# Kernel optimization log

Measured on AMD Instinct MI355X. Metric: run time of the kernel, lower is better.

## Reference

```python
import jax, jax.numpy as jnp
import numpy as np

N_NODES = 50000
N_EDGES = 800000
IN_DIM, HID_DIM, OUT_DIM = 768, 512, 256


def setup_inputs() -> dict:
    key = jax.random.key(0)
    k1, k2, k3, k4, k5 = jax.random.split(key, 5)
    x = jax.random.normal(k1, (N_NODES, IN_DIM), dtype=jnp.float32)
    edge_index = jax.random.randint(k2, (2, N_EDGES), 0, N_NODES, dtype=jnp.int64)
    # GCNConv params (glorot-ish init)
    W1 = jax.random.normal(k3, (IN_DIM, HID_DIM), dtype=jnp.float32) / np.sqrt(IN_DIM)
    b1 = jnp.zeros((HID_DIM,), dtype=jnp.float32)
    W2 = jax.random.normal(k4, (HID_DIM, OUT_DIM), dtype=jnp.float32) / np.sqrt(HID_DIM)
    b2 = jnp.zeros((OUT_DIM,), dtype=jnp.float32)
    return {"x": x, "edge_index": edge_index, "W1": W1, "b1": b1, "W2": W2, "b2": b2}


def gcn_conv(x, W, b, src, dst, n_nodes):
    """PyG GCNConv: add self-loops, symmetric degree norm, linear, scatter-add, bias."""
    h = x @ W  # [N, F_out]
    loop = jnp.arange(n_nodes, dtype=src.dtype)
    s = jnp.concatenate([src, loop])  # sources incl. self-loops
    d = jnp.concatenate([dst, loop])  # destinations incl. self-loops
    deg = jax.ops.segment_sum(jnp.ones_like(d, dtype=h.dtype), d, num_segments=n_nodes)
    dinv = jnp.where(deg > 0, jax.lax.rsqrt(deg), 0.0)
    norm = dinv[s] * dinv[d]  # [E+N]
    msgs = h[s] * norm[:, None]  # gather + scale (largest intermediate)
    out = jax.ops.segment_sum(msgs, d, num_segments=n_nodes)  # scatter-add
    return out + b


def reference(x, edge_index, W1, b1, W2, b2):
    src, dst = edge_index[0], edge_index[1]
    n = x.shape[0]
    h = gcn_conv(x, W1, b1, src, dst, n)
    h = jax.nn.relu(h)  # dropout is identity in eval mode
    out = gcn_conv(h, W2, b2, src, dst, n)
    return out
```

## Files before the change

### kernel.cpp

```cpp
#include <hip/hip_runtime.h>

#define N_NODES 50000
#define N_EDGES 800000
#define IN_DIM  768
#define HID_DIM 512
#define OUT_DIM 256
#define M_PAD   50048

typedef __attribute__((ext_vector_type(8))) short shortx8;
typedef __attribute__((ext_vector_type(4))) short shortx4;
typedef __attribute__((ext_vector_type(4))) float floatx4;

#define AS1 __attribute__((address_space(1)))
#define AS3 __attribute__((address_space(3)))

__device__ __forceinline__ unsigned short f2bf_rne(float f) {
    unsigned int u = __float_as_uint(f);
    unsigned int r = u + 0x7FFFu + ((u >> 16) & 1u);
    return (unsigned short)(r >> 16);
}
__device__ __forceinline__ float bf2f(unsigned short h) {
    return __uint_as_float(((unsigned int)h) << 16);
}

__global__ void count_deg_kernel(const int* __restrict__ dst, int* __restrict__ deg,
                                 int n_edges) {
    int e = blockIdx.x * blockDim.x + threadIdx.x;
    if (e < n_edges) atomicAdd(&deg[dst[e]], 1);
}

#define SCAN_B 256
#define N_SCAN_BLOCKS ((N_NODES + SCAN_B - 1) / SCAN_B)

__global__ void block_sum_kernel(const int* __restrict__ deg, int* __restrict__ partials,
                                 int n) {
    __shared__ int sm[SCAN_B];
    int i = blockIdx.x * SCAN_B + threadIdx.x;
    sm[threadIdx.x] = (i < n) ? deg[i] : 0;
    __syncthreads();
    for (int off = SCAN_B / 2; off > 0; off >>= 1) {
        if (threadIdx.x < off) sm[threadIdx.x] += sm[threadIdx.x + off];
        __syncthreads();
    }
    if (threadIdx.x == 0) partials[blockIdx.x] = sm[0];
}

__global__ void scan_partials_kernel(const int* __restrict__ partials,
                                     int* __restrict__ bases, int nb) {
    __shared__ int sm[SCAN_B];
    int v = (threadIdx.x < nb) ? partials[threadIdx.x] : 0;
    sm[threadIdx.x] = v;
    __syncthreads();
    for (int off = 1; off < SCAN_B; off <<= 1) {
        int t = (threadIdx.x >= off) ? sm[threadIdx.x - off] : 0;
        __syncthreads();
        sm[threadIdx.x] += t;
        __syncthreads();
    }
    if (threadIdx.x < nb) bases[threadIdx.x] = sm[threadIdx.x] - v;
}

__global__ void finalize_scan_kernel(const int* __restrict__ deg, const int* __restrict__ bases,
                                     int* __restrict__ offsets, int* __restrict__ cursor,
                                     float* __restrict__ dinv, int n) {
    __shared__ int sm[SCAN_B];
    int i = blockIdx.x * SCAN_B + threadIdx.x;
    int v = (i < n) ? deg[i] : 0;
    sm[threadIdx.x] = v;
    __syncthreads();
    for (int off = 1; off < SCAN_B; off <<= 1) {
        int t = (threadIdx.x >= off) ? sm[threadIdx.x - off] : 0;
        __syncthreads();
        sm[threadIdx.x] += t;
        __syncthreads();
    }
    if (i < n) {
        int incl = bases[blockIdx.x] + sm[threadIdx.x];
        int o = incl - v;
        offsets[i] = o;
        cursor[i]  = o;
        dinv[i]    = rsqrtf((float)(v + 1));
        if (i == n - 1) offsets[n] = incl;
    }
}

__global__ void fill_csr_kernel(const int* __restrict__ src, const int* __restrict__ dst,
                                int* __restrict__ cursor, int* __restrict__ csr_src,
                                int n_edges) {
    int e = blockIdx.x * blockDim.x + threadIdx.x;
    if (e < n_edges) {
        int p = atomicAdd(&cursor[dst[e]], 1);
        csr_src[p] = src[e];
    }
}

__global__ void convert_split_kernel(const float* __restrict__ x,
                                     unsigned short* __restrict__ xhi,
                                     unsigned short* __restrict__ xlo,
                                     long long n4) {
    long long i = (long long)blockIdx.x * blockDim.x + threadIdx.x;
    if (i >= n4) return;
    float4 v = *reinterpret_cast<const float4*>(x + i * 4);
    ushort4 h, l;
    h.x = f2bf_rne(v.x); l.x = f2bf_rne(v.x - bf2f(h.x));
    h.y = f2bf_rne(v.y); l.y = f2bf_rne(v.y - bf2f(h.y));
    h.z = f2bf_rne(v.z); l.z = f2bf_rne(v.z - bf2f(h.z));
    h.w = f2bf_rne(v.w); l.w = f2bf_rne(v.w - bf2f(h.w));
    *reinterpret_cast<ushort4*>(xhi + i * 4) = h;
    *reinterpret_cast<ushort4*>(xlo + i * 4) = l;
}

__global__ void transpose_split_kernel(const float* __restrict__ W,
                                       unsigned short* __restrict__ Whi,
                                       unsigned short* __restrict__ Wlo,
                                       int K, int N) {
    __shared__ float tile[32][33];
    int n0 = blockIdx.x * 32, k0 = blockIdx.y * 32;
    int tx = threadIdx.x, ty = threadIdx.y;
    tile[ty][tx] = W[(size_t)(k0 + ty) * N + n0 + tx];
    __syncthreads();
    float v = tile[tx][ty];
    unsigned short h = f2bf_rne(v);
    size_t o = (size_t)(n0 + ty) * K + k0 + tx;
    Whi[o] = h;
    Wlo[o] = f2bf_rne(v - bf2f(h));
}

#define GBK 32

__global__ __launch_bounds__(256)
void gemm_bf16x3_kernel(const unsigned short* __restrict__ Ahi,
                        const unsigned short* __restrict__ Alo,
                        const unsigned short* __restrict__ Bhi,
                        const unsigned short* __restrict__ Blo,
                        const float* __restrict__ dinv,
                        unsigned short* __restrict__ C,
                        int M, int N, int K) {
    __shared__ __align__(16) unsigned short As[2][2][128][GBK];
    __shared__ __align__(16) unsigned short Bs[2][2][128][GBK];

    const int tid  = threadIdx.x;
    const int lane = tid & 63;
    const int wave = tid >> 6;

    const int gx   = gridDim.x;
    const int nwg  = gx * gridDim.y;
    const int blin = blockIdx.y * gx + blockIdx.x;
    const int qq   = nwg >> 3, rr = nwg & 7;
    const int xcd  = blin & 7, idx = blin >> 3;
    const int tt   = (xcd < rr ? xcd * (qq + 1) : rr * (qq + 1) + (xcd - rr) * qq) + idx;
    const int rowBase = (tt / gx) * 128;
    const int colBase = (tt % gx) * 128;

    const unsigned short* gsrc =
        (wave == 0) ? Ahi : (wave == 1) ? Alo : (wave == 2) ? Bhi : Blo;
    unsigned short* l0 =
        (wave == 0) ? &As[0][0][0][0] : (wave == 1) ? &As[0][1][0][0]
      : (wave == 2) ? &Bs[0][0][0][0] : &Bs[0][1][0][0];
    unsigned short* l1 = l0 + 2 * 128 * GBK;
    const int rbase = (wave < 2) ? rowBase : colBase;
    const int cg = ((lane & 3) ^ ((lane >> 3) & 3)) * 8;
    const size_t laneRowOff = (size_t)(rbase + (lane >> 2)) * K + cg;

    const int m0  = (wave & 1) * 64;
    const int n0  = (wave >> 1) * 64;
    const int r16 = lane & 15;
    const int kswz = ((lane >> 4) ^ ((r16 >> 1) & 3)) * 8;

    floatx4 acc[4][4] = {};

#pragma unroll
    for (int j = 0; j < 8; j++) {
        const unsigned short* g = gsrc + laneRowOff + (size_t)(j * 16) * K;
        __builtin_amdgcn_global_load_lds((const AS1 void*)g,
                                         (AS3 void*)(l0 + j * 16 * GBK), 16, 0, 0);
    }
    __syncthreads();

    int cur = 0;
    for (int k0 = 0; k0 < K; k0 += GBK) {
        if (k0 + GBK < K) {
            unsigned short* dstp = cur ? l0 : l1;
#pragma unroll
            for (int j = 0; j < 8; j++) {
                const unsigned short* g =
                    gsrc + laneRowOff + (size_t)(j * 16) * K + (k0 + GBK);
                __builtin_amdgcn_global_load_lds((const AS1 void*)g,
                                                 (AS3 void*)(dstp + j * 16 * GBK),
                                                 16, 0, 0);
            }
        }

        shortx8 ah[4], al[4], bh[4], bv[4];
#pragma unroll
        for (int i = 0; i < 4; i++) {
            ah[i] = *reinterpret_cast<const shortx8*>(&As[cur][0][m0 + i * 16 + r16][kswz]);
            al[i] = *reinterpret_cast<const shortx8*>(&As[cur][1][m0 + i * 16 + r16][kswz]);
            bh[i] = *reinterpret_cast<const shortx8*>(&Bs[cur][0][n0 + i * 16 + r16][kswz]);
            bv[i] = *reinterpret_cast<const shortx8*>(&Bs[cur][1][n0 + i * 16 + r16][kswz]);
        }
#pragma unroll
        for (int i = 0; i < 4; i++)
#pragma unroll
            for (int j = 0; j < 4; j++) {
                acc[i][j] = __builtin_amdgcn_mfma_f32_16x16x32_bf16(ah[i], bh[j], acc[i][j], 0, 0, 0);
                acc[i][j] = __builtin_amdgcn_mfma_f32_16x16x32_bf16(ah[i], bv[j], acc[i][j], 0, 0, 0);
                acc[i][j] = __builtin_amdgcn_mfma_f32_16x16x32_bf16(al[i], bh[j], acc[i][j], 0, 0, 0);
            }
        __syncthreads();
        cur ^= 1;
    }

#pragma unroll
    for (int i = 0; i < 4; i++) {
        int rsub = rowBase + m0 + i * 16 + (lane >> 4) * 4;
#pragma unroll
        for (int j = 0; j < 4; j++) {
            int col = colBase + n0 + j * 16 + r16;
#pragma unroll
            for (int r = 0; r < 4; r++) {
                int row = rsub + r;
                if (row < M) C[(size_t)row * N + col] = f2bf_rne(acc[i][j][r] * dinv[row]);
            }
        }
    }
}

__global__ __launch_bounds__(64)
void aggregate1_kernel(const unsigned short* __restrict__ hs, const int* __restrict__ offsets,
                       const int* __restrict__ csr_src, const float* __restrict__ dinv,
                       const float* __restrict__ bias,
                       unsigned short* __restrict__ yhi,
                       unsigned short* __restrict__ ylo) {
    __shared__ int idxs[64];
    const int node = blockIdx.x;
    const int c = threadIdx.x * 8;
    const unsigned short* hp = hs + c;

    float acc[8];
    {
        shortx8 r = *reinterpret_cast<const shortx8*>(hp + (size_t)node * HID_DIM);
#pragma unroll
        for (int q = 0; q < 8; q++) acc[q] = bf2f((unsigned short)r[q]);
    }
    int beg = offsets[node], end = offsets[node + 1];
    for (int base = beg; base < end; base += 64) {
        int cnt = min(64, end - base);
        __syncthreads();
        if ((int)threadIdx.x < cnt) idxs[threadIdx.x] = csr_src[base + threadIdx.x];
        __syncthreads();
        int j = 0;
        for (; j + 8 <= cnt; j += 8) {
            shortx8 r0 = *reinterpret_cast<const shortx8*>(hp + (size_t)idxs[j + 0] * HID_DIM);
            shortx8 r1 = *reinterpret_cast<const shortx8*>(hp + (size_t)idxs[j + 1] * HID_DIM);
            shortx8 r2 = *reinterpret_cast<const shortx8*>(hp + (size_t)idxs[j + 2] * HID_DIM);
            shortx8 r3 = *reinterpret_cast<const shortx8*>(hp + (size_t)idxs[j + 3] * HID_DIM);
            shortx8 r4 = *reinterpret_cast<const shortx8*>(hp + (size_t)idxs[j + 4] * HID_DIM);
            shortx8 r5 = *reinterpret_cast<const shortx8*>(hp + (size_t)idxs[j + 5] * HID_DIM);
            shortx8 r6 = *reinterpret_cast<const shortx8*>(hp + (size_t)idxs[j + 6] * HID_DIM);
            shortx8 r7 = *reinterpret_cast<const shortx8*>(hp + (size_t)idxs[j + 7] * HID_DIM);
#pragma unroll
            for (int q = 0; q < 8; q++)
                acc[q] += ((bf2f((unsigned short)r0[q]) + bf2f((unsigned short)r1[q]))
                         + (bf2f((unsigned short)r2[q]) + bf2f((unsigned short)r3[q])))
                        + ((bf2f((unsigned short)r4[q]) + bf2f((unsigned short)r5[q]))
                         + (bf2f((unsigned short)r6[q]) + bf2f((unsigned short)r7[q])));
        }
        for (; j < cnt; j++) {
            shortx8 r = *reinterpret_cast<const shortx8*>(hp + (size_t)idxs[j] * HID_DIM);
#pragma unroll
            for (int q = 0; q < 8; q++) acc[q] += bf2f((unsigned short)r[q]);
        }
    }
    float dv = dinv[node];
    floatx4 b0 = *reinterpret_cast<const floatx4*>(bias + c);
    floatx4 b1 = *reinterpret_cast<const floatx4*>(bias + c + 4);
    shortx8 h8, l8;
#pragma unroll
    for (int q = 0; q < 8; q++) {
        float bq = (q < 4) ? b0[q] : b1[q - 4];
        float o = fmaxf(acc[q] * dv + bq, 0.f);
        unsigned short h = f2bf_rne(o);
        h8[q] = (short)h;
        l8[q] = (short)f2bf_rne(o - bf2f(h));
    }
    __builtin_nontemporal_store(h8, reinterpret_cast<shortx8*>(yhi + (size_t)node * HID_DIM + c));
    __builtin_nontemporal_store(l8, reinterpret_cast<shortx8*>(ylo + (size_t)node * HID_DIM + c));
}

__global__ __launch_bounds__(64)
void aggregate2_kernel(const unsigned short* __restrict__ hs, const int* __restrict__ offsets,
                       const int* __restrict__ csr_src, const float* __restrict__ dinv,
                       const float* __restrict__ bias, float* __restrict__ out) {
    __shared__ int idxs[64];
    const int node = blockIdx.x;
    const int c = threadIdx.x * 4;
    const unsigned short* hp = hs + c;

    float acc[4];
    {
        shortx4 r = *reinterpret_cast<const shortx4*>(hp + (size_t)node * OUT_DIM);
#pragma unroll
        for (int q = 0; q < 4; q++) acc[q] = bf2f((unsigned short)r[q]);
    }
    int beg = offsets[node], end = offsets[node + 1];
    for (int base = beg; base < end; base += 64) {
        int cnt = min(64, end - base);
        __syncthreads();
        if ((int)threadIdx.x < cnt) idxs[threadIdx.x] = csr_src[base + threadIdx.x];
        __syncthreads();
        int j = 0;
        for (; j + 8 <= cnt; j += 8) {
            shortx4 r0 = *reinterpret_cast<const shortx4*>(hp + (size_t)idxs[j + 0] * OUT_DIM);
            shortx4 r1 = *reinterpret_cast<const shortx4*>(hp + (size_t)idxs[j + 1] * OUT_DIM);
            shortx4 r2 = *reinterpret_cast<const shortx4*>(hp + (size_t)idxs[j + 2] * OUT_DIM);
            shortx4 r3 = *reinterpret_cast<const shortx4*>(hp + (size_t)idxs[j + 3] * OUT_DIM);
            shortx4 r4 = *reinterpret_cast<const shortx4*>(hp + (size_t)idxs[j + 4] * OUT_DIM);
            shortx4 r5 = *reinterpret_cast<const shortx4*>(hp + (size_t)idxs[j + 5] * OUT_DIM);
            shortx4 r6 = *reinterpret_cast<const shortx4*>(hp + (size_t)idxs[j + 6] * OUT_DIM);
            shortx4 r7 = *reinterpret_cast<const shortx4*>(hp + (size_t)idxs[j + 7] * OUT_DIM);
#pragma unroll
            for (int q = 0; q < 4; q++)
                acc[q] += ((bf2f((unsigned short)r0[q]) + bf2f((unsigned short)r1[q]))
                         + (bf2f((unsigned short)r2[q]) + bf2f((unsigned short)r3[q])))
                        + ((bf2f((unsigned short)r4[q]) + bf2f((unsigned short)r5[q]))
                         + (bf2f((unsigned short)r6[q]) + bf2f((unsigned short)r7[q])));
        }
        for (; j < cnt; j++) {
            shortx4 r = *reinterpret_cast<const shortx4*>(hp + (size_t)idxs[j] * OUT_DIM);
#pragma unroll
            for (int q = 0; q < 4; q++) acc[q] += bf2f((unsigned short)r[q]);
        }
    }
    float dv = dinv[node];
    floatx4 b = *reinterpret_cast<const floatx4*>(bias + c);
    floatx4 o = { acc[0] * dv + b[0], acc[1] * dv + b[1],
                  acc[2] * dv + b[2], acc[3] * dv + b[3] };
    __builtin_nontemporal_store(o, reinterpret_cast<floatx4*>(out + (size_t)node * OUT_DIM + c));
}

extern "C" void kernel_launch(void* const* d_in, const int* in_sizes, int n_in,
                              void* d_out, int out_size, void* d_ws, size_t ws_size,
                              hipStream_t stream) {
    const float* x    = (const float*)d_in[0];
    const int*   edge = (const int*)d_in[1];
    const float* W1   = (const float*)d_in[2];
    const float* b1   = (const float*)d_in[3];
    const float* W2   = (const float*)d_in[4];
    const float* b2   = (const float*)d_in[5];
    float* out = (float*)d_out;

    const int* src = edge;
    const int* dst = edge + N_EDGES;

    char*  ws  = (char*)d_ws;
    size_t off = 0;
    auto alloc = [&](size_t bytes) -> void* {
        void* p = ws + off;
        off += (bytes + 255) & ~(size_t)255;
        return p;
    };
    int*   deg      = (int*)alloc((size_t)N_NODES * 4);
    float* dinv     = (float*)alloc((size_t)N_NODES * 4);
    int*   offsets  = (int*)alloc((size_t)(N_NODES + 1) * 4);
    int*   cursor   = (int*)alloc((size_t)N_NODES * 4);
    int*   csr_src  = (int*)alloc((size_t)N_EDGES * 4);
    int*   partials = (int*)alloc((size_t)N_SCAN_BLOCKS * 4);
    int*   bases    = (int*)alloc((size_t)N_SCAN_BLOCKS * 4);
    unsigned short* xhi   = (unsigned short*)alloc((size_t)M_PAD * IN_DIM * 2);
    unsigned short* xlo   = (unsigned short*)alloc((size_t)M_PAD * IN_DIM * 2);
    unsigned short* w1thi = (unsigned short*)alloc((size_t)HID_DIM * IN_DIM * 2);
    unsigned short* w1tlo = (unsigned short*)alloc((size_t)HID_DIM * IN_DIM * 2);
    unsigned short* w2thi = (unsigned short*)alloc((size_t)OUT_DIM * HID_DIM * 2);
    unsigned short* w2tlo = (unsigned short*)alloc((size_t)OUT_DIM * HID_DIM * 2);
    unsigned short* hs = (unsigned short*)alloc((size_t)N_NODES * HID_DIM * 2);

    unsigned short* y1hi = xhi;
    unsigned short* y1lo = xlo;

    hipMemsetAsync(deg, 0, (size_t)N_NODES * 4, stream);
    count_deg_kernel<<<(N_EDGES + 255) / 256, 256, 0, stream>>>(dst, deg, N_EDGES);
    block_sum_kernel<<<N_SCAN_BLOCKS, SCAN_B, 0, stream>>>(deg, partials, N_NODES);
    scan_partials_kernel<<<1, SCAN_B, 0, stream>>>(partials, bases, N_SCAN_BLOCKS);
    finalize_scan_kernel<<<N_SCAN_BLOCKS, SCAN_B, 0, stream>>>(deg, bases, offsets, cursor,
                                                               dinv, N_NODES);
    fill_csr_kernel<<<(N_EDGES + 255) / 256, 256, 0, stream>>>(src, dst, cursor, csr_src, N_EDGES);

    long long n4x = (long long)N_NODES * IN_DIM / 4;
    convert_split_kernel<<<(int)((n4x + 255) / 256), 256, 0, stream>>>(x, xhi, xlo, n4x);
    transpose_split_kernel<<<dim3(HID_DIM / 32, IN_DIM / 32), dim3(32, 32), 0, stream>>>(
        W1, w1thi, w1tlo, IN_DIM, HID_DIM);
    transpose_split_kernel<<<dim3(OUT_DIM / 32, HID_DIM / 32), dim3(32, 32), 0, stream>>>(
        W2, w2thi, w2tlo, HID_DIM, OUT_DIM);

    gemm_bf16x3_kernel<<<dim3(HID_DIM / 128, M_PAD / 128), 256, 0, stream>>>(
        xhi, xlo, w1thi, w1tlo, dinv, hs, N_NODES, HID_DIM, IN_DIM);
    aggregate1_kernel<<<N_NODES, 64, 0, stream>>>(
        hs, offsets, csr_src, dinv, b1, y1hi, y1lo);

    gemm_bf16x3_kernel<<<dim3(OUT_DIM / 128, M_PAD / 128), 256, 0, stream>>>(
        y1hi, y1lo, w2thi, w2tlo, dinv, hs, N_NODES, OUT_DIM, HID_DIM);
    aggregate2_kernel<<<N_NODES, 64, 0, stream>>>(
        hs, offsets, csr_src, dinv, b2, out);
}
```

Baseline: 796.8 us.

## Load B operand directly from global into registers, halve LDS footprint

The GEMM no longer stages the weight (B) tiles through shared memory. Each wave reads its B fragments straight from global/L2 into registers every k-step, and all four waves now share the A hi/lo staging loads. Shared memory use is halved, and launch bounds request 3 blocks per CU to raise occupancy. The trade-off is that global B loads sit on the critical path with no prefetch or double-buffering, and each B element is read by two waves. That adds latency and L2 traffic, which higher occupancy may or may not hide.

```diff
diff --git a/kernel.cpp b/kernel.cpp
--- a/kernel.cpp
+++ b/kernel.cpp
@@ -128,7 +128,7 @@
 
 #define GBK 32
 
-__global__ __launch_bounds__(256)
+__global__ __launch_bounds__(256, 3)
 void gemm_bf16x3_kernel(const unsigned short* __restrict__ Ahi,
                         const unsigned short* __restrict__ Alo,
                         const unsigned short* __restrict__ Bhi,
@@ -137,7 +137,6 @@
                         unsigned short* __restrict__ C,
                         int M, int N, int K) {
     __shared__ __align__(16) unsigned short As[2][2][128][GBK];
-    __shared__ __align__(16) unsigned short Bs[2][2][128][GBK];
 
     const int tid  = threadIdx.x;
     const int lane = tid & 63;
@@ -152,52 +151,63 @@
     const int rowBase = (tt / gx) * 128;
     const int colBase = (tt % gx) * 128;
 
-    const unsigned short* gsrc =
-        (wave == 0) ? Ahi : (wave == 1) ? Alo : (wave == 2) ? Bhi : Blo;
-    unsigned short* l0 =
-        (wave == 0) ? &As[0][0][0][0] : (wave == 1) ? &As[0][1][0][0]
-      : (wave == 2) ? &Bs[0][0][0][0] : &Bs[0][1][0][0];
-    unsigned short* l1 = l0 + 2 * 128 * GBK;
-    const int rbase = (wave < 2) ? rowBase : colBase;
+    const int hl = wave >> 1;
+    const int rq = (wave & 1) * 64;
+    const unsigned short* gsrc = hl ? Alo : Ahi;
+    unsigned short* lbase = &As[0][hl][rq][0];
     const int cg = ((lane & 3) ^ ((lane >> 3) & 3)) * 8;
-    const size_t laneRowOff = (size_t)(rbase + (lane >> 2)) * K + cg;
+    const size_t laneRowOff = (size_t)(rowBase + rq + (lane >> 2)) * K + cg;
 
     const int m0  = (wave & 1) * 64;
     const int n0  = (wave >> 1) * 64;
     const int r16 = lane & 15;
+    const int kq  = (lane >> 4) * 8;
     const int kswz = ((lane >> 4) ^ ((r16 >> 1) & 3)) * 8;
 
+    const unsigned short* bph[4];
+    const unsigned short* bpl[4];
+#pragma unroll
+    for (int j = 0; j < 4; j++) {
+        int col = colBase + n0 + j * 16 + r16;
+        bph[j] = Bhi + (size_t)col * K + kq;
+        bpl[j] = Blo + (size_t)col * K + kq;
+    }
+
     floatx4 acc[4][4] = {};
 
 #pragma unroll
-    for (int j = 0; j < 8; j++) {
+    for (int j = 0; j < 4; j++) {
         const unsigned short* g = gsrc + laneRowOff + (size_t)(j * 16) * K;
         __builtin_amdgcn_global_load_lds((const AS1 void*)g,
-                                         (AS3 void*)(l0 + j * 16 * GBK), 16, 0, 0);
+                                         (AS3 void*)(lbase + j * 16 * GBK), 16, 0, 0);
     }
     __syncthreads();
 
     int cur = 0;
     for (int k0 = 0; k0 < K; k0 += GBK) {
         if (k0 + GBK < K) {
-            unsigned short* dstp = cur ? l0 : l1;
-#pragma unroll
-            for (int j = 0; j < 8; j++) {
+            unsigned short* dstb = lbase + (cur ^ 1) * (2 * 128 * GBK);
+#pragma unroll
+            for (int j = 0; j < 4; j++) {
                 const unsigned short* g =
                     gsrc + laneRowOff + (size_t)(j * 16) * K + (k0 + GBK);
                 __builtin_amdgcn_global_load_lds((const AS1 void*)g,
-                                                 (AS3 void*)(dstp + j * 16 * GBK),
+                                                 (AS3 void*)(dstb + j * 16 * GBK),
                                                  16, 0, 0);
             }
         }
 
-        shortx8 ah[4], al[4], bh[4], bv[4];
+        shortx8 bh[4], bv[4];
+#pragma unroll
+        for (int j = 0; j < 4; j++) {
+            bh[j] = *reinterpret_cast<const shortx8*>(bph[j] + k0);
+            bv[j] = *reinterpret_cast<const shortx8*>(bpl[j] + k0);
+        }
+        shortx8 ah[4], al[4];
 #pragma unroll
         for (int i = 0; i < 4; i++) {
             ah[i] = *reinterpret_cast<const shortx8*>(&As[cur][0][m0 + i * 16 + r16][kswz]);
             al[i] = *reinterpret_cast<const shortx8*>(&As[cur][1][m0 + i * 16 + r16][kswz]);
-            bh[i] = *reinterpret_cast<const shortx8*>(&Bs[cur][0][n0 + i * 16 + r16][kswz]);
-            bv[i] = *reinterpret_cast<const shortx8*>(&Bs[cur][1][n0 + i * 16 + r16][kswz]);
         }
 #pragma unroll
         for (int i = 0; i < 4; i++)
```

New measurement: 876.7 us. 1.1x slower.

## Prefetch two K-tiles ahead in the bf16x3 GEMM using explicit waitcnt barriers

Applied to the files above, without the earlier changes.

Restructures the GEMM main loop so global-to-LDS loads run two K-tiles ahead instead of one. Fragments are read from LDS into registers first, then a barrier frees that buffer so the next-next tile can be issued into it while the MFMAs run. Partial vmcnt waits replace full __syncthreads, MFMA sections get raised wave priority, and launch bounds request two workgroups per CU. The hand-written waitcnt counts assume exactly 8 outstanding loads per stage, and the occupancy hint may force register spilling.

```diff
diff --git a/kernel.cpp b/kernel.cpp
--- a/kernel.cpp
+++ b/kernel.cpp
@@ -128,7 +128,7 @@
 
 #define GBK 32
 
-__global__ __launch_bounds__(256)
+__global__ __launch_bounds__(256, 2)
 void gemm_bf16x3_kernel(const unsigned short* __restrict__ Ahi,
                         const unsigned short* __restrict__ Alo,
                         const unsigned short* __restrict__ Bhi,
@@ -154,10 +154,10 @@
 
     const unsigned short* gsrc =
         (wave == 0) ? Ahi : (wave == 1) ? Alo : (wave == 2) ? Bhi : Blo;
-    unsigned short* l0 =
+    unsigned short* lplane =
         (wave == 0) ? &As[0][0][0][0] : (wave == 1) ? &As[0][1][0][0]
       : (wave == 2) ? &Bs[0][0][0][0] : &Bs[0][1][0][0];
-    unsigned short* l1 = l0 + 2 * 128 * GBK;
+    const size_t bufStride = (size_t)2 * 128 * GBK;
     const int rbase = (wave < 2) ? rowBase : colBase;
     const int cg = ((lane & 3) ^ ((lane >> 3) & 3)) * 8;
     const size_t laneRowOff = (size_t)(rbase + (lane >> 2)) * K + cg;
@@ -168,46 +168,51 @@
     const int kswz = ((lane >> 4) ^ ((r16 >> 1) & 3)) * 8;
 
     floatx4 acc[4][4] = {};
-
-#pragma unroll
-    for (int j = 0; j < 8; j++) {
-        const unsigned short* g = gsrc + laneRowOff + (size_t)(j * 16) * K;
-        __builtin_amdgcn_global_load_lds((const AS1 void*)g,
-                                         (AS3 void*)(l0 + j * 16 * GBK), 16, 0, 0);
-    }
-    __syncthreads();
+    const int nt = K / GBK;
+
+    auto STAGE = [&](int t, int buf) {
+        unsigned short* d = lplane + (size_t)buf * bufStride;
+        const unsigned short* g = gsrc + laneRowOff + (size_t)t * GBK;
+#pragma unroll
+        for (int j = 0; j < 8; j++)
+            __builtin_amdgcn_global_load_lds((const AS1 void*)(g + (size_t)(j * 16) * K),
+                                             (AS3 void*)(d + j * 16 * GBK), 16, 0, 0);
+    };
+
+    STAGE(0, 0);
+    STAGE(1, 1);
+    asm volatile("s_waitcnt vmcnt(8)\n\ts_barrier" ::: "memory");
 
     int cur = 0;
-    for (int k0 = 0; k0 < K; k0 += GBK) {
-        if (k0 + GBK < K) {
-            unsigned short* dstp = cur ? l0 : l1;
-#pragma unroll
-            for (int j = 0; j < 8; j++) {
-                const unsigned short* g =
-                    gsrc + laneRowOff + (size_t)(j * 16) * K + (k0 + GBK);
-                __builtin_amdgcn_global_load_lds((const AS1 void*)g,
-                                                 (AS3 void*)(dstp + j * 16 * GBK),
-                                                 16, 0, 0);
-            }
-        }
-
-        shortx8 ah[4], al[4], bh[4], bv[4];
+    for (int t = 0; t < nt; ++t) {
+        shortx8 ah[4], al[4], bh[4], bl[4];
 #pragma unroll
         for (int i = 0; i < 4; i++) {
             ah[i] = *reinterpret_cast<const shortx8*>(&As[cur][0][m0 + i * 16 + r16][kswz]);
             al[i] = *reinterpret_cast<const shortx8*>(&As[cur][1][m0 + i * 16 + r16][kswz]);
             bh[i] = *reinterpret_cast<const shortx8*>(&Bs[cur][0][n0 + i * 16 + r16][kswz]);
-            bv[i] = *reinterpret_cast<const shortx8*>(&Bs[cur][1][n0 + i * 16 + r16][kswz]);
-        }
+            bl[i] = *reinterpret_cast<const shortx8*>(&Bs[cur][1][n0 + i * 16 + r16][kswz]);
+        }
+        asm volatile("s_waitcnt lgkmcnt(0)\n\ts_barrier" ::: "memory");
+        __builtin_amdgcn_sched_barrier(0);
+        if (t + 2 < nt) STAGE(t + 2, cur);
+
+        __builtin_amdgcn_s_setprio(1);
 #pragma unroll
         for (int i = 0; i < 4; i++)
 #pragma unroll
             for (int j = 0; j < 4; j++) {
                 acc[i][j] = __builtin_amdgcn_mfma_f32_16x16x32_bf16(ah[i], bh[j], acc[i][j], 0, 0, 0);
-                acc[i][j] = __builtin_amdgcn_mfma_f32_16x16x32_bf16(ah[i], bv[j], acc[i][j], 0, 0, 0);
+                acc[i][j] = __builtin_amdgcn_mfma_f32_16x16x32_bf16(ah[i], bl[j], acc[i][j], 0, 0, 0);
                 acc[i][j] = __builtin_amdgcn_mfma_f32_16x16x32_bf16(al[i], bh[j], acc[i][j], 0, 0, 0);
             }
-        __syncthreads();
+        __builtin_amdgcn_s_setprio(0);
+
+        if (t + 1 < nt) {
+            if (t + 2 < nt) asm volatile("s_waitcnt vmcnt(8)\n\ts_barrier" ::: "memory");
+            else            asm volatile("s_waitcnt vmcnt(0)\n\ts_barrier" ::: "memory");
+            __builtin_amdgcn_sched_barrier(0);
+        }
         cur ^= 1;
     }
 
```

New measurement: 792.6 us. Within noise of the previous version (-0.5%).
